# Performance work log

Hardware: AMD Instinct MI355X
Metric: run time of the kernel (lower is better)

Reference implementation:

```python
import jax, jax.numpy as jnp
import numpy as np

B, S, E, FF, Q = 8, 2048, 768, 3072, 8  # batch, seq, embed_dim, ffn_dim, n_qubits


def setup_inputs() -> dict:
    key = jax.random.key(0)
    k_x, k_phi, k_w1, k_w2 = jax.random.split(key, 4)
    x = jax.random.normal(k_x, (B, S, E), dtype=jnp.float32)
    # trainable RY angles (one per qubit), like tq.RY(has_params=True)
    phi = jax.random.normal(k_phi, (Q,), dtype=jnp.float32)
    # linear1: n_qubits -> ffn_dim ; linear2: ffn_dim -> embed_dim (torch layout [out, in])
    w1 = jax.random.normal(k_w1, (FF, Q), dtype=jnp.float32) / np.sqrt(Q).astype(np.float32)
    b1 = jnp.zeros((FF,), dtype=jnp.float32)
    w2 = jax.random.normal(k_w2, (E, FF), dtype=jnp.float32) / np.sqrt(FF).astype(np.float32)
    b2 = jnp.zeros((E,), dtype=jnp.float32)
    return {"x": x, "phi": phi, "w1": w1, "b1": b1, "w2": w2, "b2": b2}


def reference(x, phi, w1, b1, w2, b2):
    # Quantum block (exact closed form): for each token, encoder applies
    # RY(x_i) on wire i, then a trainable RY(phi_i) on wire i. Starting from
    # |0>^Q this is a product state; RY compose additively and
    # <Z> after RY(theta)|0> == cos(theta). MeasureAll(PauliZ) therefore gives:
    n_qubits = phi.shape[0]
    meas = jnp.cos(x[..., :n_qubits] + phi)          # [B, S, Q]
    # dropout is identity in eval mode
    h = jax.nn.relu(jnp.einsum('bsq,fq->bsf', meas, w1) + b1)  # [B, S, FF]
    return jnp.einsum('bsf,ef->bse', h, w2) + b2               # [B, S, E]
```

## Files before the change

kernel.cpp:

```cpp
#include <hip/hip_runtime.h>
#include <hip/hip_bf16.h>
#include <stdint.h>

#define M_TOK 16384
#define E_DIM 768
#define FF_DIM 3072
#define Q_N 8

typedef __attribute__((ext_vector_type(8))) short bf16x8;
typedef __attribute__((ext_vector_type(4))) float f32x4;

__device__ inline unsigned short f2bf(float f) {
  union { float f; unsigned u; } v; v.f = f;
  unsigned r = v.u + 0x7fffu + ((v.u >> 16) & 1u);
  return (unsigned short)(r >> 16);
}

__global__ __launch_bounds__(256) void cvt_w2(const float* __restrict__ w2,
                                              __hip_bfloat16* __restrict__ w2b) {
  int i = (blockIdx.x * 256 + threadIdx.x) * 4;
  const int n = E_DIM * FF_DIM;
  if (i < n) {
    float4 v = *(const float4*)(w2 + i);
    ushort4 o;
    o.x = f2bf(v.x); o.y = f2bf(v.y); o.z = f2bf(v.z); o.w = f2bf(v.w);
    *(ushort4*)((unsigned short*)w2b + i) = o;
  }
}

__global__ __launch_bounds__(256) void compute_h(const float* __restrict__ x,
                                                 const float* __restrict__ phi,
                                                 const float* __restrict__ w1,
                                                 const float* __restrict__ b1,
                                                 __hip_bfloat16* __restrict__ hout) {
  __shared__ float s_meas[32][8];
  const int t = threadIdx.x;
  const int bm = blockIdx.x / 6;
  const int bf = blockIdx.x % 6;
  const int m0 = bm * 32;
  const int f0 = bf * 512;

  if (t < 64) {
    int m = t >> 1, hh = t & 1;
    float4 v = *(const float4*)(x + (size_t)(m0 + m) * E_DIM + hh * 4);
    float4 p = *(const float4*)(phi + hh * 4);
    s_meas[m][hh * 4 + 0] = __cosf(v.x + p.x);
    s_meas[m][hh * 4 + 1] = __cosf(v.y + p.y);
    s_meas[m][hh * 4 + 2] = __cosf(v.z + p.z);
    s_meas[m][hh * 4 + 3] = __cosf(v.w + p.w);
  }
  __syncthreads();

  const float4* wr = (const float4*)(w1 + (size_t)(f0 + 2 * t) * Q_N);
  float4 a0 = wr[0], a1 = wr[1], b0 = wr[2], b1v = wr[3];
  float wA[8] = {a0.x, a0.y, a0.z, a0.w, a1.x, a1.y, a1.z, a1.w};
  float wB[8] = {b0.x, b0.y, b0.z, b0.w, b1v.x, b1v.y, b1v.z, b1v.w};
  const float biasA = b1[f0 + 2 * t];
  const float biasB = b1[f0 + 2 * t + 1];

  uint32_t* dst32 = (uint32_t*)hout;
  for (int m = 0; m < 32; ++m) {
    float a = biasA, b = biasB;
#pragma unroll
    for (int q = 0; q < 8; ++q) {
      float mv = s_meas[m][q];
      a = fmaf(mv, wA[q], a);
      b = fmaf(mv, wB[q], b);
    }
    a = fmaxf(a, 0.f);
    b = fmaxf(b, 0.f);
    uint32_t pack = (uint32_t)f2bf(a) | ((uint32_t)f2bf(b) << 16);
    dst32[(size_t)(m0 + m) * (FF_DIM / 2) + (f0 / 2) + t] = pack;
  }
}

#define GLDS16(g, l)                                                          \
  __builtin_amdgcn_global_load_lds(                                           \
      (const __attribute__((address_space(1))) void*)(g),                     \
      (__attribute__((address_space(3))) void*)(l), 16, 0, 0)

#define BUF_ELEMS 20480
#define B_OFF 8192

__global__ __launch_bounds__(256, 2) void gemm_bt(const __hip_bfloat16* __restrict__ A,
                                                  const __hip_bfloat16* __restrict__ Bw,
                                                  const float* __restrict__ b2,
                                                  float* __restrict__ C) {
  const int K = FF_DIM;
  const int N = E_DIM;

  __shared__ __align__(16) __hip_bfloat16 lds[2 * BUF_ELEMS];

  const int t = threadIdx.x;
  const int swz = (blockIdx.x & 7) * 64 + (blockIdx.x >> 3);
  const int bm = swz >> 2;
  const int bn = swz & 3;
  const size_t m0 = (size_t)bm * 128;
  const int n0 = bn * 192;

  const int w = t >> 6, l = t & 63;
  const int wr = w >> 1;
  const int wc = w & 1;
  const int lr = l & 15;
  const int lk = l >> 4;

  const int x0 = lk ^ (lr & 7);
  const int x1 = x0 ^ 4;
  const int baseA = (wr * 64 + lr) * 64;
  const int baseB = B_OFF + (wc * 96 + lr) * 64;
  const int offA0 = baseA + x0 * 8, offA1 = baseA + x1 * 8;
  const int offB0 = baseB + x0 * 8, offB1 = baseB + x1 * 8;

  const int rs = t >> 3;
  const int lc = (t & 7) ^ (rs & 7);
  const __hip_bfloat16* sA[4];
  const __hip_bfloat16* sB[6];
#pragma unroll
  for (int s = 0; s < 4; ++s) sA[s] = A + (m0 + s * 32 + rs) * (size_t)K + lc * 8;
#pragma unroll
  for (int s = 0; s < 6; ++s) sB[s] = Bw + ((size_t)n0 + s * 32 + rs) * K + lc * 8;

  f32x4 acc[4][6] = {};

#define STAGE(K0S, WBUF)                                                      \
  {                                                                           \
    __hip_bfloat16* ld = lds + (WBUF) * BUF_ELEMS + t * 8;                    \
    GLDS16(sA[0] + (K0S), ld);                                                \
    GLDS16(sA[1] + (K0S), ld + 2048);                                         \
    GLDS16(sA[2] + (K0S), ld + 4096);                                         \
    GLDS16(sA[3] + (K0S), ld + 6144);                                         \
    GLDS16(sB[0] + (K0S), ld + 8192);                                         \
    GLDS16(sB[1] + (K0S), ld + 10240);                                        \
    GLDS16(sB[2] + (K0S), ld + 12288);                                        \
    GLDS16(sB[3] + (K0S), ld + 14336);                                        \
    GLDS16(sB[4] + (K0S), ld + 16384);                                        \
    GLDS16(sB[5] + (K0S), ld + 18432);                                        \
  }

#define TILE(KT, RBUF, DO_STAGE)                                              \
  {                                                                           \
    if (DO_STAGE) STAGE(((KT) + 1) * 64, (RBUF) ^ 1);                         \
    const __hip_bfloat16* la = lds + (RBUF) * BUF_ELEMS;                      \
    {                                                 \
      bf16x8 fa[4], fb[6];                                                    \
      _Pragma("unroll") for (int mi = 0; mi < 4; ++mi)                        \
          fa[mi] = *(const bf16x8*)(la + offA0 + mi * 1024);                  \
      _Pragma("unroll") for (int ni = 0; ni < 6; ++ni)                        \
          fb[ni] = *(const bf16x8*)(la + offB0 + ni * 1024);                  \
      __builtin_amdgcn_s_setprio(1);                                          \
      _Pragma("unroll") for (int mi = 0; mi < 4; ++mi)                        \
          _Pragma("unroll") for (int ni = 0; ni < 6; ++ni)                    \
              acc[mi][ni] = __builtin_amdgcn_mfma_f32_16x16x32_bf16(          \
                  fa[mi], fb[ni], acc[mi][ni], 0, 0, 0);                      \
      __builtin_amdgcn_s_setprio(0);                                          \
    }                                                                         \
    {                                                 \
      bf16x8 fa[4], fb[6];                                                    \
      _Pragma("unroll") for (int mi = 0; mi < 4; ++mi)                        \
          fa[mi] = *(const bf16x8*)(la + offA1 + mi * 1024);                  \
      _Pragma("unroll") for (int ni = 0; ni < 6; ++ni)                        \
          fb[ni] = *(const bf16x8*)(la + offB1 + ni * 1024);                  \
      __builtin_amdgcn_s_setprio(1);                                          \
      _Pragma("unroll") for (int mi = 0; mi < 4; ++mi)                        \
          _Pragma("unroll") for (int ni = 0; ni < 6; ++ni)                    \
              acc[mi][ni] = __builtin_amdgcn_mfma_f32_16x16x32_bf16(          \
                  fa[mi], fb[ni], acc[mi][ni], 0, 0, 0);                      \
      __builtin_amdgcn_s_setprio(0);                                          \
    }                                                                         \
    asm volatile("s_waitcnt vmcnt(0)" ::: "memory");                          \
    __builtin_amdgcn_s_barrier();                                             \
  }

  STAGE(0, 0);
  asm volatile("s_waitcnt vmcnt(0)" ::: "memory");
  __builtin_amdgcn_s_barrier();

#pragma unroll 1
  for (int tt = 0; tt < 46; tt += 2) {
    TILE(tt + 0, 0, 1);
    TILE(tt + 1, 1, 1);
  }
  TILE(46, 0, 1);
  TILE(47, 1, 0);

#undef TILE
#undef STAGE

#pragma unroll
  for (int mi = 0; mi < 4; ++mi) {
    const size_t row = m0 + wr * 64 + mi * 16 + lk * 4;
#pragma unroll
    for (int ni = 0; ni < 6; ++ni) {
      const int col = n0 + wc * 96 + ni * 16 + lr;
      const float bias = b2[col];
#pragma unroll
      for (int rr = 0; rr < 4; ++rr) {
        C[(row + rr) * N + col] = acc[mi][ni][rr] + bias;
      }
    }
  }
}

__global__ __launch_bounds__(256) void fallback_fused(const float* __restrict__ x,
                                                      const float* __restrict__ phi,
                                                      const float* __restrict__ w1,
                                                      const float* __restrict__ b1,
                                                      const float* __restrict__ w2,
                                                      const float* __restrict__ b2,
                                                      float* __restrict__ out) {
  __shared__ float s_h[FF_DIM];
  __shared__ float s_meas[Q_N];
  const int t = threadIdx.x;
  const size_t m = blockIdx.x;
  if (t < Q_N) s_meas[t] = __cosf(x[m * E_DIM + t] + phi[t]);
  __syncthreads();
  for (int f = t; f < FF_DIM; f += 256) {
    const float4* wr = (const float4*)(w1 + (size_t)f * Q_N);
    float4 a = wr[0], b = wr[1];
    float acc = b1[f];
    acc = fmaf(s_meas[0], a.x, acc); acc = fmaf(s_meas[1], a.y, acc);
    acc = fmaf(s_meas[2], a.z, acc); acc = fmaf(s_meas[3], a.w, acc);
    acc = fmaf(s_meas[4], b.x, acc); acc = fmaf(s_meas[5], b.y, acc);
    acc = fmaf(s_meas[6], b.z, acc); acc = fmaf(s_meas[7], b.w, acc);
    s_h[f] = fmaxf(acc, 0.f);
  }
  __syncthreads();
  for (int e = t; e < E_DIM; e += 256) {
    const float* w2r = w2 + (size_t)e * FF_DIM;
    float acc = b2[e];
    for (int f = 0; f < FF_DIM; f += 4) {
      float4 wv = *(const float4*)(w2r + f);
      acc = fmaf(s_h[f + 0], wv.x, acc);
      acc = fmaf(s_h[f + 1], wv.y, acc);
      acc = fmaf(s_h[f + 2], wv.z, acc);
      acc = fmaf(s_h[f + 3], wv.w, acc);
    }
    out[m * E_DIM + e] = acc;
  }
}

extern "C" void kernel_launch(void* const* d_in, const int* in_sizes, int n_in,
                              void* d_out, int out_size, void* d_ws, size_t ws_size,
                              hipStream_t stream) {
  const float* x   = (const float*)d_in[0];
  const float* phi = (const float*)d_in[1];
  const float* w1  = (const float*)d_in[2];
  const float* b1  = (const float*)d_in[3];
  const float* w2  = (const float*)d_in[4];
  const float* b2  = (const float*)d_in[5];
  float* out = (float*)d_out;

  const size_t H_BYTES   = (size_t)M_TOK * FF_DIM * 2;
  const size_t W2B_BYTES = (size_t)E_DIM * FF_DIM * 2;
  const size_t NEED = H_BYTES + W2B_BYTES;

  if (ws_size >= NEED) {
    __hip_bfloat16* h   = (__hip_bfloat16*)d_ws;
    __hip_bfloat16* w2b = (__hip_bfloat16*)((char*)d_ws + H_BYTES);
    cvt_w2<<<(E_DIM * FF_DIM) / (256 * 4), 256, 0, stream>>>(w2, w2b);
    compute_h<<<(M_TOK / 32) * (FF_DIM / 512), 256, 0, stream>>>(x, phi, w1, b1, h);
    gemm_bt<<<(M_TOK / 128) * (E_DIM / 192), 256, 0, stream>>>(h, w2b, b2, out);
  } else {
    fallback_fused<<<M_TOK, 256, 0, stream>>>(x, phi, w1, b1, w2, b2, out);
  }
}
```

Measured before the change: 104.3 us.

## Triple-buffer LDS and prefetch next tile's fragments across barrier in GEMM

```diff
diff --git a/kernel.cpp b/kernel.cpp
--- a/kernel.cpp
+++ b/kernel.cpp
@@ -82,14 +82,14 @@
 #define BUF_ELEMS 20480
 #define B_OFF 8192
 
-__global__ __launch_bounds__(256, 2) void gemm_bt(const __hip_bfloat16* __restrict__ A,
+__global__ __launch_bounds__(256, 1) void gemm_bt(const __hip_bfloat16* __restrict__ A,
                                                   const __hip_bfloat16* __restrict__ Bw,
                                                   const float* __restrict__ b2,
                                                   float* __restrict__ C) {
   const int K = FF_DIM;
   const int N = E_DIM;
 
-  __shared__ __align__(16) __hip_bfloat16 lds[2 * BUF_ELEMS];
+  __shared__ __align__(16) __hip_bfloat16 lds[3 * BUF_ELEMS];
 
   const int t = threadIdx.x;
   const int swz = (blockIdx.x & 7) * 64 + (blockIdx.x >> 3);
@@ -137,53 +137,71 @@
     GLDS16(sB[5] + (K0S), ld + 18432);                                        \
   }
 
-#define TILE(KT, RBUF, DO_STAGE)                                              \
+#define RD_K0(DA, DB, LA)                                                     \
+  _Pragma("unroll") for (int mi = 0; mi < 4; ++mi)                            \
+      DA[mi] = *(const bf16x8*)((LA) + offA0 + mi * 1024);                    \
+  _Pragma("unroll") for (int ni = 0; ni < 6; ++ni)                            \
+      DB[ni] = *(const bf16x8*)((LA) + offB0 + ni * 1024);
+
+#define RD_K1(DA, DB, LA)                                                     \
+  _Pragma("unroll") for (int mi = 0; mi < 4; ++mi)                            \
+      DA[mi] = *(const bf16x8*)((LA) + offA1 + mi * 1024);                    \
+  _Pragma("unroll") for (int ni = 0; ni < 6; ++ni)                            \
+      DB[ni] = *(const bf16x8*)((LA) + offB1 + ni * 1024);
+
+#define MFMA_BLK(FA, FB)                                                      \
+  _Pragma("unroll") for (int mi = 0; mi < 4; ++mi)                            \
+    _Pragma("unroll") for (int ni = 0; ni < 6; ++ni)                          \
+      acc[mi][ni] = __builtin_amdgcn_mfma_f32_16x16x32_bf16(                  \
+          FA[mi], FB[ni], acc[mi][ni], 0, 0, 0);
+
+#define TILE(KT, RBCUR, RBNXT, RBSTG, CA, CB, NA, NB, DO_STAGE, DO_NEXT)      \
   {                                                                           \
-    if (DO_STAGE) STAGE(((KT) + 1) * 64, (RBUF) ^ 1);                         \
-    const __hip_bfloat16* la = lds + (RBUF) * BUF_ELEMS;                      \
-    {                                                 \
-      bf16x8 fa[4], fb[6];                                                    \
-      _Pragma("unroll") for (int mi = 0; mi < 4; ++mi)                        \
-          fa[mi] = *(const bf16x8*)(la + offA0 + mi * 1024);                  \
-      _Pragma("unroll") for (int ni = 0; ni < 6; ++ni)                        \
-          fb[ni] = *(const bf16x8*)(la + offB0 + ni * 1024);                  \
-      __builtin_amdgcn_s_setprio(1);                                          \
-      _Pragma("unroll") for (int mi = 0; mi < 4; ++mi)                        \
-          _Pragma("unroll") for (int ni = 0; ni < 6; ++ni)                    \
-              acc[mi][ni] = __builtin_amdgcn_mfma_f32_16x16x32_bf16(          \
-                  fa[mi], fb[ni], acc[mi][ni], 0, 0, 0);                      \
-      __builtin_amdgcn_s_setprio(0);                                          \
-    }                                                                         \
-    {                                                 \
-      bf16x8 fa[4], fb[6];                                                    \
-      _Pragma("unroll") for (int mi = 0; mi < 4; ++mi)                        \
-          fa[mi] = *(const bf16x8*)(la + offA1 + mi * 1024);                  \
-      _Pragma("unroll") for (int ni = 0; ni < 6; ++ni)                        \
-          fb[ni] = *(const bf16x8*)(la + offB1 + ni * 1024);                  \
-      __builtin_amdgcn_s_setprio(1);                                          \
-      _Pragma("unroll") for (int mi = 0; mi < 4; ++mi)                        \
-          _Pragma("unroll") for (int ni = 0; ni < 6; ++ni)                    \
-              acc[mi][ni] = __builtin_amdgcn_mfma_f32_16x16x32_bf16(          \
-                  fa[mi], fb[ni], acc[mi][ni], 0, 0, 0);                      \
-      __builtin_amdgcn_s_setprio(0);                                          \
-    }                                                                         \
-    asm volatile("s_waitcnt vmcnt(0)" ::: "memory");                          \
+    const __hip_bfloat16* lcur = lds + (RBCUR) * BUF_ELEMS;                   \
+    const __hip_bfloat16* lnxt = lds + (RBNXT) * BUF_ELEMS;                   \
+    if (DO_STAGE) STAGE(((KT) + 2) * 64, (RBSTG));                            \
+    bf16x8 fa1[4], fb1[6];                                                    \
+    RD_K1(fa1, fb1, lcur);                                                    \
+    __builtin_amdgcn_s_setprio(1);                                            \
+    MFMA_BLK(CA, CB);                     \
+    __builtin_amdgcn_s_setprio(0);                                            \
+    if (DO_STAGE) { asm volatile("s_waitcnt vmcnt(10)" ::: "memory"); }       \
+    else          { asm volatile("s_waitcnt vmcnt(0)"  ::: "memory"); }       \
+    __builtin_amdgcn_s_barrier();          \
+    if (DO_NEXT) { RD_K0(NA, NB, lnxt); }                                     \
+    __builtin_amdgcn_s_setprio(1);                                            \
+    MFMA_BLK(fa1, fb1);                                                       \
+    __builtin_amdgcn_s_setprio(0);                                            \
     __builtin_amdgcn_s_barrier();                                             \
   }
 
   STAGE(0, 0);
   asm volatile("s_waitcnt vmcnt(0)" ::: "memory");
   __builtin_amdgcn_s_barrier();
+  bf16x8 pa[4], pb[6], qa[4], qb[6];
+  RD_K0(pa, pb, lds);
+  STAGE(64, 1);
 
 #pragma unroll 1
-  for (int tt = 0; tt < 46; tt += 2) {
-    TILE(tt + 0, 0, 1);
-    TILE(tt + 1, 1, 1);
-  }
-  TILE(46, 0, 1);
-  TILE(47, 1, 0);
+  for (int tt = 0; tt < 42; tt += 6) {
+    TILE(tt + 0, 0, 1, 2, pa, pb, qa, qb, 1, 1);
+    TILE(tt + 1, 1, 2, 0, qa, qb, pa, pb, 1, 1);
+    TILE(tt + 2, 2, 0, 1, pa, pb, qa, qb, 1, 1);
+    TILE(tt + 3, 0, 1, 2, qa, qb, pa, pb, 1, 1);
+    TILE(tt + 4, 1, 2, 0, pa, pb, qa, qb, 1, 1);
+    TILE(tt + 5, 2, 0, 1, qa, qb, pa, pb, 1, 1);
+  }
+  TILE(42, 0, 1, 2, pa, pb, qa, qb, 1, 1);
+  TILE(43, 1, 2, 0, qa, qb, pa, pb, 1, 1);
+  TILE(44, 2, 0, 1, pa, pb, qa, qb, 1, 1);
+  TILE(45, 0, 1, 2, qa, qb, pa, pb, 1, 1);
+  TILE(46, 1, 2, 0, pa, pb, qa, qb, 0, 1);
+  TILE(47, 2, 0, 1, qa, qb, pa, pb, 0, 0);
 
 #undef TILE
+#undef MFMA_BLK
+#undef RD_K0
+#undef RD_K1
 #undef STAGE
 
 #pragma unroll
```

New measurement: 113.1 us. +8.5%, slower.

## Pre-pack W2 into MFMA fragment layout and load B directly to registers

Applied to the files above, without the earlier changes.

```diff
diff --git a/kernel.cpp b/kernel.cpp
--- a/kernel.cpp
+++ b/kernel.cpp
@@ -16,16 +16,24 @@
   return (unsigned short)(r >> 16);
 }
 
-__global__ __launch_bounds__(256) void cvt_w2(const float* __restrict__ w2,
-                                              __hip_bfloat16* __restrict__ w2b) {
-  int i = (blockIdx.x * 256 + threadIdx.x) * 4;
-  const int n = E_DIM * FF_DIM;
-  if (i < n) {
-    float4 v = *(const float4*)(w2 + i);
-    ushort4 o;
-    o.x = f2bf(v.x); o.y = f2bf(v.y); o.z = f2bf(v.z); o.w = f2bf(v.w);
-    *(ushort4*)((unsigned short*)w2b + i) = o;
-  }
+__global__ __launch_bounds__(256) void cvt_w2f(const float* __restrict__ w2,
+                                               __hip_bfloat16* __restrict__ w2f) {
+  const int tid = blockIdx.x * 256 + threadIdx.x;
+  const int l = tid & 63;
+  const int fid = tid >> 6;
+  const int nt = fid % 48;
+  const int kth = fid / 48;
+  const int col = nt * 16 + (l & 15);
+  const int k0 = kth * 32 + ((l >> 4) << 3);
+  const float* src = w2 + (size_t)col * FF_DIM + k0;
+  float4 v0 = *(const float4*)(src);
+  float4 v1 = *(const float4*)(src + 4);
+  uint4 o;
+  o.x = (uint32_t)f2bf(v0.x) | ((uint32_t)f2bf(v0.y) << 16);
+  o.y = (uint32_t)f2bf(v0.z) | ((uint32_t)f2bf(v0.w) << 16);
+  o.z = (uint32_t)f2bf(v1.x) | ((uint32_t)f2bf(v1.y) << 16);
+  o.w = (uint32_t)f2bf(v1.z) | ((uint32_t)f2bf(v1.w) << 16);
+  *(uint4*)((unsigned short*)w2f + (size_t)tid * 8) = o;
 }
 
 __global__ __launch_bounds__(256) void compute_h(const float* __restrict__ x,
@@ -79,17 +87,16 @@
       (const __attribute__((address_space(1))) void*)(g),                     \
       (__attribute__((address_space(3))) void*)(l), 16, 0, 0)
 
-#define BUF_ELEMS 20480
-#define B_OFF 8192
+#define A_ELEMS 8192
 
 __global__ __launch_bounds__(256, 2) void gemm_bt(const __hip_bfloat16* __restrict__ A,
-                                                  const __hip_bfloat16* __restrict__ Bw,
+                                                  const __hip_bfloat16* __restrict__ w2f,
                                                   const float* __restrict__ b2,
                                                   float* __restrict__ C) {
   const int K = FF_DIM;
   const int N = E_DIM;
 
-  __shared__ __align__(16) __hip_bfloat16 lds[2 * BUF_ELEMS];
+  __shared__ __align__(16) __hip_bfloat16 lds[2 * A_ELEMS];
 
   const int t = threadIdx.x;
   const int swz = (blockIdx.x & 7) * 64 + (blockIdx.x >> 3);
@@ -98,100 +105,102 @@
   const size_t m0 = (size_t)bm * 128;
   const int n0 = bn * 192;
 
-  const int w = t >> 6, l = t & 63;
-  const int wr = w >> 1;
-  const int wc = w & 1;
+  const int wc = t >> 6;
+  const int l = t & 63;
   const int lr = l & 15;
   const int lk = l >> 4;
 
   const int x0 = lk ^ (lr & 7);
   const int x1 = x0 ^ 4;
-  const int baseA = (wr * 64 + lr) * 64;
-  const int baseB = B_OFF + (wc * 96 + lr) * 64;
-  const int offA0 = baseA + x0 * 8, offA1 = baseA + x1 * 8;
-  const int offB0 = baseB + x0 * 8, offB1 = baseB + x1 * 8;
+  const int offA0 = lr * 64 + x0 * 8;
+  const int offA1 = lr * 64 + x1 * 8;
 
   const int rs = t >> 3;
   const int lc = (t & 7) ^ (rs & 7);
   const __hip_bfloat16* sA[4];
-  const __hip_bfloat16* sB[6];
 #pragma unroll
   for (int s = 0; s < 4; ++s) sA[s] = A + (m0 + s * 32 + rs) * (size_t)K + lc * 8;
-#pragma unroll
-  for (int s = 0; s < 6; ++s) sB[s] = Bw + ((size_t)n0 + s * 32 + rs) * K + lc * 8;
-
-  f32x4 acc[4][6] = {};
-
-#define STAGE(K0S, WBUF)                                                      \
+
+  const __hip_bfloat16* fb = w2f + ((size_t)(bn * 12 + wc * 3)) * 512 + l * 8;
+
+  f32x4 acc[8][3] = {};
+  bf16x8 BA[6], BB[6];
+
+#define STAGE_A(K0S, WBUF)                                                    \
   {                                                                           \
-    __hip_bfloat16* ld = lds + (WBUF) * BUF_ELEMS + t * 8;                    \
+    __hip_bfloat16* ld = lds + (WBUF) * A_ELEMS + t * 8;                      \
     GLDS16(sA[0] + (K0S), ld);                                                \
     GLDS16(sA[1] + (K0S), ld + 2048);                                         \
     GLDS16(sA[2] + (K0S), ld + 4096);                                         \
     GLDS16(sA[3] + (K0S), ld + 6144);                                         \
-    GLDS16(sB[0] + (K0S), ld + 8192);                                         \
-    GLDS16(sB[1] + (K0S), ld + 10240);                                        \
-    GLDS16(sB[2] + (K0S), ld + 12288);                                        \
-    GLDS16(sB[3] + (K0S), ld + 14336);                                        \
-    GLDS16(sB[4] + (K0S), ld + 16384);                                        \
-    GLDS16(sB[5] + (K0S), ld + 18432);                                        \
-  }
-
-#define TILE(KT, RBUF, DO_STAGE)                                              \
+  }
+
+#define LOADB(DST, KT)                                                        \
+  _Pragma("unroll") for (int j = 0; j < 6; ++j)                               \
+      DST[j] = *(const bf16x8*)(fb + ((size_t)((KT) * 2 + (j / 3)) * 24576) + \
+                                (j % 3) * 512);
+
+#define TILE(KT, RBUF, BCUR, BNXT, DO_NEXT)                                   \
   {                                                                           \
-    if (DO_STAGE) STAGE(((KT) + 1) * 64, (RBUF) ^ 1);                         \
-    const __hip_bfloat16* la = lds + (RBUF) * BUF_ELEMS;                      \
-    {                                                 \
-      bf16x8 fa[4], fb[6];                                                    \
-      _Pragma("unroll") for (int mi = 0; mi < 4; ++mi)                        \
-          fa[mi] = *(const bf16x8*)(la + offA0 + mi * 1024);                  \
-      _Pragma("unroll") for (int ni = 0; ni < 6; ++ni)                        \
-          fb[ni] = *(const bf16x8*)(la + offB0 + ni * 1024);                  \
+    if (DO_NEXT) STAGE_A(((KT) + 1) * 64, (RBUF) ^ 1);                        \
+    __builtin_amdgcn_sched_barrier(0);                                        \
+    if (DO_NEXT) LOADB(BNXT, (KT) + 1);                                       \
+    __builtin_amdgcn_sched_barrier(0);                                        \
+    const __hip_bfloat16* la = lds + (RBUF) * A_ELEMS;                        \
+    {                                                           \
+      bf16x8 a[8];                                                            \
+      _Pragma("unroll") for (int mi = 0; mi < 8; ++mi)                        \
+          a[mi] = *(const bf16x8*)(la + offA0 + mi * 1024);                   \
       __builtin_amdgcn_s_setprio(1);                                          \
-      _Pragma("unroll") for (int mi = 0; mi < 4; ++mi)                        \
-          _Pragma("unroll") for (int ni = 0; ni < 6; ++ni)                    \
+      _Pragma("unroll") for (int mi = 0; mi < 8; ++mi)                        \
+          _Pragma("unroll") for (int ni = 0; ni < 3; ++ni)                    \
               acc[mi][ni] = __builtin_amdgcn_mfma_f32_16x16x32_bf16(          \
-                  fa[mi], fb[ni], acc[mi][ni], 0, 0, 0);                      \
+                  a[mi], BCUR[ni], acc[mi][ni], 0, 0, 0);                     \
       __builtin_amdgcn_s_setprio(0);                                          \
     }                                                                         \
-    {                                                 \
-      bf16x8 fa[4], fb[6];                                                    \
-      _Pragma("unroll") for (int mi = 0; mi < 4; ++mi)                        \
-          fa[mi] = *(const bf16x8*)(la + offA1 + mi * 1024);                  \
-      _Pragma("unroll") for (int ni = 0; ni < 6; ++ni)                        \
-          fb[ni] = *(const bf16x8*)(la + offB1 + ni * 1024);                  \
+    {                                                           \
+      bf16x8 a[8];                                                            \
+      _Pragma("unroll") for (int mi = 0; mi < 8; ++mi)                        \
+          a[mi] = *(const bf16x8*)(la + offA1 + mi * 1024);                   \
       __builtin_amdgcn_s_setprio(1);                                          \
-      _Pragma("unroll") for (int mi = 0; mi < 4; ++mi)                        \
-          _Pragma("unroll") for (int ni = 0; ni < 6; ++ni)                    \
+      _Pragma("unroll") for (int mi = 0; mi < 8; ++mi)                        \
+          _Pragma("unroll") for (int ni = 0; ni < 3; ++ni)                    \
               acc[mi][ni] = __builtin_amdgcn_mfma_f32_16x16x32_bf16(          \
-                  fa[mi], fb[ni], acc[mi][ni], 0, 0, 0);                      \
+                  a[mi], BCUR[3 + ni], acc[mi][ni], 0, 0, 0);                 \
       __builtin_amdgcn_s_setprio(0);                                          \
     }                                                                         \
-    asm volatile("s_waitcnt vmcnt(0)" ::: "memory");                          \
-    __builtin_amdgcn_s_barrier();                                             \
-  }
-
-  STAGE(0, 0);
-  asm volatile("s_waitcnt vmcnt(0)" ::: "memory");
+    if (DO_NEXT) {                                                            \
+      __builtin_amdgcn_sched_barrier(0);                                      \
+      asm volatile("s_waitcnt vmcnt(6)" ::: "memory");     \
+      __builtin_amdgcn_s_barrier();                                           \
+    }                                                                         \
+  }
+
+  STAGE_A(0, 0);
+  __builtin_amdgcn_sched_barrier(0);
+  LOADB(BA, 0);
+  __builtin_amdgcn_sched_barrier(0);
+  asm volatile("s_waitcnt vmcnt(6)" ::: "memory");
   __builtin_amdgcn_s_barrier();
 
 #pragma unroll 1
   for (int tt = 0; tt < 46; tt += 2) {
-    TILE(tt + 0, 0, 1);
-    TILE(tt + 1, 1, 1);
-  }
-  TILE(46, 0, 1);
-  TILE(47, 1, 0);
+    TILE(tt + 0, 0, BA, BB, 1);
+    TILE(tt + 1, 1, BB, BA, 1);
+  }
+  TILE(46, 0, BA, BB, 1);
+  TILE(47, 1, BB, BA, 0);
 
 #undef TILE
-#undef STAGE
-
-#pragma unroll
-  for (int mi = 0; mi < 4; ++mi) {
-    const size_t row = m0 + wr * 64 + mi * 16 + lk * 4;
-#pragma unroll
-    for (int ni = 0; ni < 6; ++ni) {
-      const int col = n0 + wc * 96 + ni * 16 + lr;
+#undef LOADB
+#undef STAGE_A
+
+#pragma unroll
+  for (int mi = 0; mi < 8; ++mi) {
+    const size_t row = m0 + mi * 16 + lk * 4;
+#pragma unroll
+    for (int ni = 0; ni < 3; ++ni) {
+      const int col = n0 + wc * 48 + ni * 16 + lr;
       const float bias = b2[col];
 #pragma unroll
       for (int rr = 0; rr < 4; ++rr) {
@@ -251,15 +260,15 @@
   float* out = (float*)d_out;
 
   const size_t H_BYTES   = (size_t)M_TOK * FF_DIM * 2;
-  const size_t W2B_BYTES = (size_t)E_DIM * FF_DIM * 2;
-  const size_t NEED = H_BYTES + W2B_BYTES;
+  const size_t W2F_BYTES = (size_t)E_DIM * FF_DIM * 2;
+  const size_t NEED = H_BYTES + W2F_BYTES;
 
   if (ws_size >= NEED) {
     __hip_bfloat16* h   = (__hip_bfloat16*)d_ws;
-    __hip_bfloat16* w2b = (__hip_bfloat16*)((char*)d_ws + H_BYTES);
-    cvt_w2<<<(E_DIM * FF_DIM) / (256 * 4), 256, 0, stream>>>(w2, w2b);
+    __hip_bfloat16* w2f = (__hip_bfloat16*)((char*)d_ws + H_BYTES);
+    cvt_w2f<<<1152, 256, 0, stream>>>(w2, w2f);
     compute_h<<<(M_TOK / 32) * (FF_DIM / 512), 256, 0, stream>>>(x, phi, w1, b1, h);
-    gemm_bt<<<(M_TOK / 128) * (E_DIM / 192), 256, 0, stream>>>(h, w2b, b2, out);
+    gemm_bt<<<(M_TOK / 128) * (E_DIM / 192), 256, 0, stream>>>(h, w2f, b2, out);
   } else {
     fallback_fused<<<M_TOK, 256, 0, stream>>>(x, phi, w1, b1, w2, b2, out);
   }
```

New measurement: 103.6 us. No clear change (-0.7%).
